# Performance work log

Hardware: AMD Instinct MI355X
Metric: run time of the kernel (lower is better)

The kernel has to match this reference:

```python
import jax, jax.numpy as jnp
import numpy as np

B, N_PER, P_PER = 64, 64, 2016   # graphs, nodes/graph, pairs/graph (C(64,2))
IN_DIM, HID, OUT = 64, 128, 10
EDGE_P = 0.125


def _build_graph_structures():
    """Integer preprocessing replicating build_2sets_from_embeddings's
    combinatorics (pairs, iso_type source, triangle-based 2-set edges)."""
    rng = np.random.default_rng(0)
    n, b = N_PER, B
    A = rng.random((b, n, n)) < EDGE_P
    A = np.triu(A, 1)
    A = A | A.transpose(0, 2, 1)                      # symmetric, no self loops
    gs, us, vs = np.nonzero(A)                        # directed edges, both dirs
    edge_index = np.stack([gs * n + us, gs * n + vs]).astype(np.int64)
    batch = np.repeat(np.arange(b), n).astype(np.int64)
    iu, iv = np.triu_indices(n, 1)                    # local pair (u<v) lists
    pidx = np.full((n, n), -1, np.int64)
    pidx[iu, iv] = np.arange(P_PER)
    pidx[iv, iu] = np.arange(P_PER)                   # symmetric lookup = sorted()
    pair_u = (np.arange(b)[:, None] * n + iu[None, :]).ravel().astype(np.int64)
    pair_v = (np.arange(b)[:, None] * n + iv[None, :]).ravel().astype(np.int64)
    iso_type = A[:, iu, iv].astype(np.float32).ravel()[:, None]  # [B*P_PER,1]
    # 2-set edges: pair (u,v) -> sorted(v,w) and sorted(u,w) for every common
    # neighbor w of u and v (matches _build_2set_edges exactly)
    common = A[:, iu, :] & A[:, iv, :]                # (B, P_PER, n)
    g2, ps, ws = np.nonzero(common)
    u, v = iu[ps], iv[ps]
    d1 = pidx[v, ws]
    d2 = pidx[u, ws]
    src = np.concatenate([g2 * P_PER + ps, g2 * P_PER + ps])
    dst = np.concatenate([g2 * P_PER + d1, g2 * P_PER + d2])
    two_edges = np.stack([src, dst]).astype(np.int64)
    two_batch = np.repeat(np.arange(b), P_PER).astype(np.int64)
    return edge_index, batch, pair_u, pair_v, iso_type, two_edges, two_batch


def setup_inputs() -> dict:
    ei, batch, pu, pv, iso, te, tb = _build_graph_structures()
    key = jax.random.key(0)
    ks = jax.random.split(key, 16)
    w = lambda k, i, o: jax.random.normal(k, (i, o), jnp.float32) / np.float32(np.sqrt(i))
    two_in = 2 * HID + 1
    return {
        "x": jax.random.normal(ks[0], (B * N_PER, IN_DIM), jnp.float32),
        "g1_W1_0": w(ks[1], IN_DIM, HID), "g1_W2_0": w(ks[2], IN_DIM, HID),
        "g1_W1_1": w(ks[3], HID, HID),    "g1_W2_1": w(ks[4], HID, HID),
        "g1_W1_2": w(ks[5], HID, HID),    "g1_W2_2": w(ks[6], HID, HID),
        "k_W1_0": w(ks[7], two_in, HID),  "k_W2_0": w(ks[8], two_in, HID),
        "k_W1_1": w(ks[9], HID, HID),     "k_W2_1": w(ks[10], HID, HID),
        "c_W0": w(ks[11], 2 * HID, HID),  "c_b0": jnp.zeros((HID,), jnp.float32),
        "c_W1": w(ks[12], HID, OUT),      "c_b1": jnp.zeros((OUT,), jnp.float32),
        "iso_type": jnp.asarray(iso),
        "edge_index": jnp.asarray(ei), "batch": jnp.asarray(batch),
        "pair_u": jnp.asarray(pu), "pair_v": jnp.asarray(pv),
        "two_edges": jnp.asarray(te), "two_batch": jnp.asarray(tb),
    }


def _mp_layer(h, ei, W1, W2):
    # relu( h @ W1 + scatter_add_{dst}( h[src] @ W2 ) )  -- OneGNNLayer / KSetLayer
    msg = h[ei[0]] @ W2
    agg = jax.ops.segment_sum(msg, ei[1], num_segments=h.shape[0])
    return jax.nn.relu(h @ W1 + agg)


def reference(x, g1_W1_0, g1_W2_0, g1_W1_1, g1_W2_1, g1_W1_2, g1_W2_2,
              k_W1_0, k_W2_0, k_W1_1, k_W2_1,
              c_W0, c_b0, c_W1, c_b1,
              iso_type, edge_index, batch, pair_u, pair_v, two_edges, two_batch):
    h = _mp_layer(x, edge_index, g1_W1_0, g1_W2_0)
    h = _mp_layer(h, edge_index, g1_W1_1, g1_W2_1)
    h = _mp_layer(h, edge_index, g1_W1_2, g1_W2_2)
    graph_emb_1 = jax.ops.segment_sum(h, batch, num_segments=B)
    # 2-set features: [h_u, h_v, iso_type]  -> [P, 2H+1]
    two_x = jnp.concatenate([h[pair_u], h[pair_v], iso_type], axis=1)
    h2 = _mp_layer(two_x, two_edges, k_W1_0, k_W2_0)
    h2 = _mp_layer(h2, two_edges, k_W1_1, k_W2_1)
    graph_emb_2 = jax.ops.segment_sum(h2, two_batch, num_segments=B)
    combined = jnp.concatenate([graph_emb_1, graph_emb_2], axis=1)
    hc = jax.nn.relu(combined @ c_W0 + c_b0)   # Dropout(p=0.5) inactive in eval
    return hc @ c_W1 + c_b1
```

## Files before the change

### kernel.cpp

```cpp
#include <hip/hip_runtime.h>
#include <hip/hip_bf16.h>


typedef short s16x8 __attribute__((ext_vector_type(8)));
typedef float f32x4 __attribute__((ext_vector_type(4)));

__device__ __forceinline__ unsigned short f2bf(float f) {
  union { float f; unsigned u; } x; x.f = f;
  unsigned r = (x.u + 0x7fffu + ((x.u >> 16) & 1u)) >> 16;
  return (unsigned short)r;
}
__device__ __forceinline__ float bf2f(unsigned short h) {
  union { unsigned u; float f; } x; x.u = ((unsigned)h) << 16;
  return x.f;
}
__device__ __forceinline__ float4 ldbf4(const unsigned short* p) {
  ushort4 q = *(const ushort4*)p;
  return make_float4(bf2f(q.x), bf2f(q.y), bf2f(q.z), bf2f(q.w));
}
__device__ __forceinline__ void stbf4(unsigned short* p, float4 v) {
  ushort4 q;
  q.x = f2bf(v.x); q.y = f2bf(v.y); q.z = f2bf(v.z); q.w = f2bf(v.w);
  *(ushort4*)p = q;
}
__device__ __forceinline__ float4 ld4(const float* p) { return *(const float4*)p; }

template<int KCS, int ASTR>
__device__ __forceinline__ void mfma_dual_lds(
    const unsigned short* A, const unsigned short* Wfrag,
    f32x4 (&accA)[8], f32x4 (&accB)[8])
{
  const int lane = threadIdx.x & 63;
  const int wv = threadIdx.x >> 6;
  const int row = wv * 16 + (lane & 15);
  const int k0 = (lane >> 4) << 3;
  const unsigned short* ap = A + row * ASTR + k0;
  const unsigned short* wp = Wfrag + (size_t)lane * 8;
#pragma unroll
  for (int i = 0; i < 8; ++i) { accA[i] = (f32x4)0.f; accB[i] = (f32x4)0.f; }
#pragma unroll
  for (int kc = 0; kc < KCS; ++kc) {
    s16x8 af = *(const s16x8*)(ap + kc * 32);
#pragma unroll
    for (int nt = 0; nt < 8; ++nt) {
      s16x8 b0 = *(const s16x8*)(wp + ((size_t)((nt)*KCS + kc) << 9));
      s16x8 b1 = *(const s16x8*)(wp + ((size_t)((8 + nt) * KCS + kc) << 9));
      accA[nt] = __builtin_amdgcn_mfma_f32_16x16x32_bf16(af, b0, accA[nt], 0, 0, 0);
      accB[nt] = __builtin_amdgcn_mfma_f32_16x16x32_bf16(af, b1, accB[nt], 0, 0, 0);
    }
  }
}

template<int KCS, int ASTR>
__device__ __forceinline__ void mfma_dual_lds16(
    const unsigned short* A, const unsigned short* Wfrag,
    f32x4 (&accA)[2], f32x4 (&accB)[2])
{
  const int lane = threadIdx.x & 63;
  const int w16 = threadIdx.x >> 6;
  const int rw = w16 & 3, ch = w16 >> 2;
  const int row = rw * 16 + (lane & 15);
  const int k0 = (lane >> 4) << 3;
  const unsigned short* ap = A + row * ASTR + k0;
  const unsigned short* wp = Wfrag + (size_t)lane * 8;
  accA[0] = (f32x4)0.f; accA[1] = (f32x4)0.f;
  accB[0] = (f32x4)0.f; accB[1] = (f32x4)0.f;
  __builtin_amdgcn_s_setprio(1);
#pragma unroll
  for (int kc = 0; kc < KCS; ++kc) {
    s16x8 af = *(const s16x8*)(ap + kc * 32);
#pragma unroll
    for (int n2 = 0; n2 < 2; ++n2) {
      int nt = ch * 2 + n2;
      s16x8 b0 = *(const s16x8*)(wp + ((size_t)(nt * KCS + kc) << 9));
      s16x8 b1 = *(const s16x8*)(wp + ((size_t)((8 + nt) * KCS + kc) << 9));
      accA[n2] = __builtin_amdgcn_mfma_f32_16x16x32_bf16(af, b0, accA[n2], 0, 0, 0);
      accB[n2] = __builtin_amdgcn_mfma_f32_16x16x32_bf16(af, b1, accB[n2], 0, 0, 0);
    }
  }
  __builtin_amdgcn_s_setprio(0);
}

__device__ __forceinline__ void epi_lds16(const f32x4 (&accA)[2], const f32x4 (&accB)[2],
    unsigned short (*preS)[136], unsigned short (*msgS)[136])
{
  const int lane = threadIdx.x & 63;
  const int w16 = threadIdx.x >> 6;
  const int rw = w16 & 3, ch = w16 >> 2;
  const int col = lane & 15;
  const int r0 = rw * 16 + ((lane >> 4) << 2);
  __syncthreads();
#pragma unroll
  for (int n2 = 0; n2 < 2; ++n2) {
    int nt = ch * 2 + n2;
#pragma unroll
    for (int r = 0; r < 4; ++r) {
      preS[r0 + r][nt * 16 + col] = f2bf(accA[n2][r]);
      msgS[r0 + r][nt * 16 + col] = f2bf(accB[n2][r]);
    }
  }
  __syncthreads();
}

__device__ __forceinline__ void epi_global(const f32x4 (&accA)[8], const f32x4 (&accB)[8],
    unsigned short (*sOut)[136], unsigned short* Ca, unsigned short* Cb, long tile)
{
  const int tid = threadIdx.x;
  const int lane = tid & 63;
  const int wv = tid >> 6;
  const int col = lane & 15;
  const int r0 = wv * 16 + ((lane >> 4) << 2);
  const long rowBase = tile * 64;
#pragma unroll
  for (int sel = 0; sel < 2; ++sel) {
    __syncthreads();
#pragma unroll
    for (int nt = 0; nt < 8; ++nt) {
#pragma unroll
      for (int r = 0; r < 4; ++r)
        sOut[r0 + r][nt * 16 + col] = f2bf(sel ? accB[nt][r] : accA[nt][r]);
    }
    __syncthreads();
    unsigned short* C = sel ? Cb : Ca;
#pragma unroll
    for (int i = 0; i < 4; ++i) {
      int fi = tid + i * 256;
      int row = fi >> 4;
      int c8 = fi & 15;
      *(uint4*)(C + (rowBase + row) * 128 + c8 * 8) = *(uint4*)&sOut[row][c8 * 8];
    }
  }
}

struct NArgs {
  const float* x;
  const int* ei;
  const int* gstart;
  const unsigned short *Wf0, *Wf1, *Wf2;
  unsigned short* Hn;
  float* ge1;
  int E1;
  const int* degP;
  int* bsumP;
  int P;
};

__global__ __launch_bounds__(1024) void node_plus(NArgs a)
{
  __shared__ __align__(16) unsigned short hS[64][136];
  __shared__ __align__(16) unsigned short preS[64][136];
  __shared__ __align__(16) unsigned short msgS[64][136];
  __shared__ int ldeg[64], lcur[64], loff[65];
  __shared__ unsigned short ledge[1024];
  __shared__ float sge[128];
  __shared__ int rs[1024];

  const int t = threadIdx.x;

  if ((int)blockIdx.x >= 64) {
    int chunk = blockIdx.x - 64;
    int idx = chunk * 1024 + t;
    rs[t] = (idx < a.P) ? a.degP[idx] : 0;
    __syncthreads();
    for (int d = 512; d > 0; d >>= 1) {
      if (t < d) rs[t] += rs[t + d];
      __syncthreads();
    }
    if (t == 0) a.bsumP[chunk] = rs[0];
    return;
  }

  const int b = blockIdx.x;
  const int base = b * 64;

  const int es = a.gstart[b], ee = a.gstart[b + 1];
  if (t < 64) ldeg[t] = 0;
  if (t < 128) sge[t] = 0.f;
  __syncthreads();
  for (int i = es + t; i < ee; i += 1024)
    atomicAdd(&ldeg[a.ei[a.E1 + i] - base], 1);
  __syncthreads();
  if (t < 64) {
    int v = ldeg[t], s = v;
#pragma unroll
    for (int d = 1; d < 64; d <<= 1) {
      int o = __shfl_up(s, d, 64);
      if (t >= d) s += o;
    }
    loff[t] = s - v;
    lcur[t] = s - v;
    if (t == 63) loff[64] = s;
  }
  unsigned short* xs = &preS[0][0];
  for (int i = t; i < 64 * 64; i += 1024) {
    int r = i >> 6, c = i & 63;
    xs[r * 72 + c] = f2bf(a.x[(size_t)(base + r) * 64 + c]);
  }
  __syncthreads();
  for (int i = es + t; i < ee; i += 1024) {
    int s = a.ei[i] - base, d = a.ei[a.E1 + i] - base;
    int pos = atomicAdd(&lcur[d], 1);
    ledge[pos] = (unsigned short)s;
  }
  __syncthreads();

  f32x4 accA[2], accB[2];
  const int grp = t >> 5, f = (t & 31) * 4;

  mfma_dual_lds16<2, 72>(xs, a.Wf0, accA, accB);
  epi_lds16(accA, accB, preS, msgS);
  for (int r = grp; r < 64; r += 32) {
    float4 acc = ldbf4(&preS[r][f]);
    int j1 = loff[r + 1];
    for (int j = loff[r]; j < j1; ++j) {
      float4 m = ldbf4(&msgS[ledge[j]][f]);
      acc.x += m.x; acc.y += m.y; acc.z += m.z; acc.w += m.w;
    }
    stbf4(&hS[r][f], make_float4(fmaxf(acc.x, 0.f), fmaxf(acc.y, 0.f),
                                 fmaxf(acc.z, 0.f), fmaxf(acc.w, 0.f)));
  }
  __syncthreads();

  mfma_dual_lds16<4, 136>(&hS[0][0], a.Wf1, accA, accB);
  epi_lds16(accA, accB, preS, msgS);
  for (int r = grp; r < 64; r += 32) {
    float4 acc = ldbf4(&preS[r][f]);
    int j1 = loff[r + 1];
    for (int j = loff[r]; j < j1; ++j) {
      float4 m = ldbf4(&msgS[ledge[j]][f]);
      acc.x += m.x; acc.y += m.y; acc.z += m.z; acc.w += m.w;
    }
    stbf4(&hS[r][f], make_float4(fmaxf(acc.x, 0.f), fmaxf(acc.y, 0.f),
                                 fmaxf(acc.z, 0.f), fmaxf(acc.w, 0.f)));
  }
  __syncthreads();

  mfma_dual_lds16<4, 136>(&hS[0][0], a.Wf2, accA, accB);
  epi_lds16(accA, accB, preS, msgS);
  {
    float4 g = make_float4(0.f, 0.f, 0.f, 0.f);
    for (int r = grp; r < 64; r += 32) {
      float4 acc = ldbf4(&preS[r][f]);
      int j1 = loff[r + 1];
      for (int j = loff[r]; j < j1; ++j) {
        float4 m = ldbf4(&msgS[ledge[j]][f]);
        acc.x += m.x; acc.y += m.y; acc.z += m.z; acc.w += m.w;
      }
      float4 o = make_float4(fmaxf(acc.x, 0.f), fmaxf(acc.y, 0.f),
                             fmaxf(acc.z, 0.f), fmaxf(acc.w, 0.f));
      stbf4(&hS[r][f], o);
      g.x += o.x; g.y += o.y; g.z += o.z; g.w += o.w;
    }
    atomicAdd(&sge[f + 0], g.x);
    atomicAdd(&sge[f + 1], g.y);
    atomicAdd(&sge[f + 2], g.z);
    atomicAdd(&sge[f + 3], g.w);
  }
  __syncthreads();
  if (t < 128) a.ge1[b * 128 + t] = sge[t];
  {
    int row = t >> 4, c8 = t & 15;
    *(uint4*)(a.Hn + (size_t)(base + row) * 128 + c8 * 8) = *(uint4*)&hS[row][c8 * 8];
  }
}

struct HArgs {
  const unsigned short* Hn;
  const unsigned short *Wf3, *Wf4;
  unsigned short *HU1, *HU2, *HV1, *HV2;
  const int* degP;
  const int* bsumP;
  int* offP; int* curP;
  int P; int nb;
};

__global__ __launch_bounds__(256) void hv_plus(HArgs a)
{
  __shared__ __align__(16) unsigned short hS[64][136];
  __shared__ int s[256];
  __shared__ int basePfx;
  const int tid = threadIdx.x;

  if ((int)blockIdx.x >= 128) {
    int b = blockIdx.x - 128;
    int t = tid;
    if (t == 0) {
      int acc = 0;
      for (int k = 0; k < b; ++k) acc += a.bsumP[k];
      basePfx = acc;
    }
    int base = b * 1024 + t * 4;
    int v0 = 0, v1 = 0, v2 = 0, v3 = 0;
    if (base + 0 < a.P) v0 = a.degP[base + 0];
    if (base + 1 < a.P) v1 = a.degP[base + 1];
    if (base + 2 < a.P) v2 = a.degP[base + 2];
    if (base + 3 < a.P) v3 = a.degP[base + 3];
    s[t] = v0 + v1 + v2 + v3;
    __syncthreads();
    for (int d = 1; d < 256; d <<= 1) {
      int v = (t >= d) ? s[t - d] : 0;
      __syncthreads();
      s[t] += v;
      __syncthreads();
    }
    int run = basePfx + ((t == 0) ? 0 : s[t - 1]);
    if (base + 0 < a.P) { a.offP[base + 0] = run; a.curP[base + 0] = run; run += v0; }
    if (base + 1 < a.P) { a.offP[base + 1] = run; a.curP[base + 1] = run; run += v1; }
    if (base + 2 < a.P) { a.offP[base + 2] = run; a.curP[base + 2] = run; run += v2; }
    if (base + 3 < a.P) { a.offP[base + 3] = run; a.curP[base + 3] = run; run += v3; }
    if (b == a.nb - 1 && t == 0) a.offP[a.P] = basePfx + a.bsumP[b];
    return;
  }

  const int g = blockIdx.x >> 1;
  const int sel = blockIdx.x & 1;
  const unsigned short* src = a.Hn + (size_t)g * 64 * 128;
#pragma unroll
  for (int i = 0; i < 4; ++i) {
    int fi = tid + i * 256;
    int row = fi >> 4, c8 = fi & 15;
    *(uint4*)&hS[row][c8 * 8] = *(const uint4*)(src + row * 128 + c8 * 8);
  }
  __syncthreads();
  f32x4 accA[8], accB[8];
  mfma_dual_lds<4, 136>(&hS[0][0], sel ? a.Wf4 : a.Wf3, accA, accB);
  epi_global(accA, accB, hS, sel ? a.HV1 : a.HU1, sel ? a.HV2 : a.HU2, g);
}

struct PrepArgs {
  const float* wa[6];
  const float* wb[6];
  unsigned short* Wf[6];
  const int* te; int E2;
  int* degP;
  const int* ei; int E1;
  int* gstart;
  int nCnt;
};

__global__ void prep(PrepArgs p)
{
  int bb = blockIdx.x, t = threadIdx.x;
  if (bb < 88) {
    int gid = bb * 256 + t;
    if (gid < 22528) {
      int pi, local, kcs, kclog;
      if (gid < 2048) { pi = 0; local = gid; kcs = 2; kclog = 1; }
      else { int r = gid - 2048; pi = 1 + (r >> 12); local = r & 4095; kcs = 4; kclog = 2; }
      int lane = local & 63;
      int t1 = local >> 6;
      int kc = t1 & (kcs - 1);
      int t2 = t1 >> kclog;
      int nt = t2 & 7;
      int wsel = t2 >> 3;
      const float* W = wsel ? p.wb[pi] : p.wa[pi];
      int k0 = kc * 32 + ((lane >> 4) << 3);
      int n = nt * 16 + (lane & 15);
      unsigned short tmp[8];
#pragma unroll
      for (int j = 0; j < 8; ++j) tmp[j] = f2bf(W[(size_t)(k0 + j) * 128 + n]);
      *(uint4*)(p.Wf[pi] + (size_t)local * 8) = *(uint4*)tmp;
    }
  } else if (bb < 88 + p.nCnt) {
    int e = (bb - 88) * 256 + t;
    if (e < p.E2) atomicAdd(&p.degP[p.te[p.E2 + e]], 1);
  } else {
    int e = (bb - 88 - p.nCnt) * 256 + t;
    if (e <= p.E1) {
      int ge = (e < p.E1) ? (p.ei[e] >> 6) : 64;
      int gp = (e > 0) ? (p.ei[e - 1] >> 6) : -1;
      for (int g = gp + 1; g <= ge; ++g) p.gstart[g] = e;
    }
  }
}

__global__ void csr_fill_pair(const int* __restrict__ te, int E2,
                              const int* __restrict__ pu, const int* __restrict__ pv,
                              const float* __restrict__ iso,
                              int* __restrict__ curP, int4* __restrict__ recP)
{
  int e = blockIdx.x * 256 + threadIdx.x;
  if (e >= E2) return;
  int s = te[e], d = te[E2 + e];
  int pos = atomicAdd(&curP[d], 1);
  recP[pos] = make_int4(pu[s], pv[s], __float_as_int(iso[s]), s);
}

__global__ __launch_bounds__(256) void gather_two0_bf(
    const unsigned short* __restrict__ HU1, const unsigned short* __restrict__ HV1,
    const unsigned short* __restrict__ HU2, const unsigned short* __restrict__ HV2,
    const float* __restrict__ iso,
    const float* __restrict__ w1iso, const float* __restrict__ w2iso,
    const int* __restrict__ pu, const int* __restrict__ pv,
    const int* __restrict__ off, const int4* __restrict__ rec,
    unsigned short* __restrict__ out, int P)
{
  int blk = (int)blockIdx.x;
  const int nB = (int)gridDim.x;
  if ((nB & 7) == 0)
    blk = (blk & 7) * (nB >> 3) + (blk >> 3);
  int p = blk * 8 + (threadIdx.x >> 5);
  if (p >= P) return;
  int f = (threadIdx.x & 31) * 4;
  float4 wi1 = ld4(w1iso + f);
  float4 wi2 = ld4(w2iso + f);
  int u0 = pu[p], v0 = pv[p];
  float is0 = iso[p];
  float4 a = ldbf4(HU1 + (size_t)u0 * 128 + f);
  float4 b = ldbf4(HV1 + (size_t)v0 * 128 + f);
  float4 acc;
  acc.x = a.x + b.x + is0 * wi1.x;
  acc.y = a.y + b.y + is0 * wi1.y;
  acc.z = a.z + b.z + is0 * wi1.z;
  acc.w = a.w + b.w + is0 * wi1.w;
  int j = off[p], e1 = off[p + 1];
  for (; j + 1 < e1; j += 2) {
    int4 r0 = rec[j], r1 = rec[j + 1];
    float4 mu0 = ldbf4(HU2 + (size_t)r0.x * 128 + f);
    float4 mv0 = ldbf4(HV2 + (size_t)r0.y * 128 + f);
    float4 mu1 = ldbf4(HU2 + (size_t)r1.x * 128 + f);
    float4 mv1 = ldbf4(HV2 + (size_t)r1.y * 128 + f);
    float i0 = __int_as_float(r0.z), i1 = __int_as_float(r1.z);
    acc.x += mu0.x + mv0.x + i0 * wi2.x + mu1.x + mv1.x + i1 * wi2.x;
    acc.y += mu0.y + mv0.y + i0 * wi2.y + mu1.y + mv1.y + i1 * wi2.y;
    acc.z += mu0.z + mv0.z + i0 * wi2.z + mu1.z + mv1.z + i1 * wi2.z;
    acc.w += mu0.w + mv0.w + i0 * wi2.w + mu1.w + mv1.w + i1 * wi2.w;
  }
  if (j < e1) {
    int4 r0 = rec[j];
    float4 mu0 = ldbf4(HU2 + (size_t)r0.x * 128 + f);
    float4 mv0 = ldbf4(HV2 + (size_t)r0.y * 128 + f);
    float i0 = __int_as_float(r0.z);
    acc.x += mu0.x + mv0.x + i0 * wi2.x;
    acc.y += mu0.y + mv0.y + i0 * wi2.y;
    acc.z += mu0.z + mv0.z + i0 * wi2.z;
    acc.w += mu0.w + mv0.w + i0 * wi2.w;
  }
  stbf4(out + (size_t)p * 128 + f,
        make_float4(fmaxf(acc.x, 0.f), fmaxf(acc.y, 0.f),
                    fmaxf(acc.z, 0.f), fmaxf(acc.w, 0.f)));
}

__global__ __launch_bounds__(64) void pair_l1(
    const unsigned short* __restrict__ H2,
    const unsigned short* __restrict__ Wfrag,
    const int* __restrict__ off, const int4* __restrict__ rec,
    float* __restrict__ gep)
{
  __shared__ __align__(16) unsigned short hS[16][136];
  __shared__ int offS[17];
  __shared__ int recwS[256];
  __shared__ float sge[128];

  const int tid = threadIdx.x;
  int qt = (int)blockIdx.x;
  const int nB = (int)gridDim.x;
  if ((nB & 7) == 0)
    qt = (qt & 7) * (nB >> 3) + (qt >> 3);
  const int r0 = qt * 16;

  if (tid < 17) offS[tid] = off[r0 + tid];
  sge[tid] = 0.f;
  sge[tid + 64] = 0.f;

  {
    const unsigned short* src = H2 + (size_t)r0 * 128;
#pragma unroll
    for (int i = 0; i < 4; ++i) {
      int fi = tid + i * 64;
      int row = fi >> 4, c8 = fi & 15;
      *(uint4*)&hS[row][c8 * 8] = *(const uint4*)(src + row * 128 + c8 * 8);
    }
  }
  __syncthreads();

  const int e0 = offS[0];
  const int ecnt = offS[16] - e0;
  const bool useS = (ecnt <= 256);
  if (useS)
    for (int j = tid; j < ecnt; j += 64) recwS[j] = rec[e0 + j].w;

  const int lane = tid;
  const int arow = lane & 15;
  const int k0 = (lane >> 4) << 3;
  const unsigned short* hp = &hS[0][0] + arow * 136 + k0;
  const unsigned short* wp = Wfrag + (size_t)lane * 8;
  f32x4 acc[8];
#pragma unroll
  for (int nt = 0; nt < 8; ++nt) acc[nt] = (f32x4)0.f;
  __builtin_amdgcn_s_setprio(1);
#pragma unroll
  for (int kc = 0; kc < 4; ++kc) {
    s16x8 ah = *(const s16x8*)(hp + kc * 32);
#pragma unroll
    for (int nt = 0; nt < 8; ++nt) {
      s16x8 b0 = *(const s16x8*)(wp + ((size_t)(nt * 4 + kc) << 9));
      acc[nt] = __builtin_amdgcn_mfma_f32_16x16x32_bf16(ah, b0, acc[nt], 0, 0, 0);
    }
  }
  __builtin_amdgcn_s_setprio(0);
  __syncthreads();

  {
    const int grp = tid >> 5, f = (tid & 31) * 4;
    for (int i = grp; i < 16; i += 2) {
      float4 a = make_float4(0.f, 0.f, 0.f, 0.f);
      int j = offS[i], e1 = offS[i + 1];
      for (; j + 1 < e1; j += 2) {
        int s0 = useS ? recwS[j - e0] : rec[j].w;
        int s1 = useS ? recwS[j + 1 - e0] : rec[j + 1].w;
        float4 m0 = ldbf4(H2 + (size_t)s0 * 128 + f);
        float4 m1 = ldbf4(H2 + (size_t)s1 * 128 + f);
        a.x += m0.x + m1.x; a.y += m0.y + m1.y;
        a.z += m0.z + m1.z; a.w += m0.w + m1.w;
      }
      if (j < e1) {
        int s0 = useS ? recwS[j - e0] : rec[j].w;
        float4 m0 = ldbf4(H2 + (size_t)s0 * 128 + f);
        a.x += m0.x; a.y += m0.y; a.z += m0.z; a.w += m0.w;
      }
      stbf4(&hS[i][f], a);
    }
  }
  __syncthreads();

  __builtin_amdgcn_s_setprio(1);
#pragma unroll
  for (int kc = 0; kc < 4; ++kc) {
    s16x8 ag = *(const s16x8*)(hp + kc * 32);
#pragma unroll
    for (int nt = 0; nt < 8; ++nt) {
      s16x8 b1 = *(const s16x8*)(wp + ((size_t)((8 + nt) * 4 + kc) << 9));
      acc[nt] = __builtin_amdgcn_mfma_f32_16x16x32_bf16(ag, b1, acc[nt], 0, 0, 0);
    }
  }
  __builtin_amdgcn_s_setprio(0);

  const int col0 = lane & 15;
#pragma unroll
  for (int nt = 0; nt < 8; ++nt) {
    float s = fmaxf(acc[nt][0], 0.f) + fmaxf(acc[nt][1], 0.f)
            + fmaxf(acc[nt][2], 0.f) + fmaxf(acc[nt][3], 0.f);
    atomicAdd(&sge[nt * 16 + col0], s);
  }
  __syncthreads();
  gep[(size_t)qt * 128 + tid] = sge[tid];
  gep[(size_t)qt * 128 + tid + 64] = sge[tid + 64];
}

__global__ void classifier(const float* __restrict__ ge1, const float* __restrict__ gep,
                           const float* __restrict__ W0, const float* __restrict__ b0,
                           const float* __restrict__ W1, const float* __restrict__ b1,
                           float* __restrict__ out)
{
  __shared__ float comb[256];
  __shared__ float hc[128];
  int g = blockIdx.x, t = threadIdx.x;
  comb[t] = ge1[g * 128 + t];
  float s2 = 0.f;
  const float* gpr = gep + (size_t)g * 126 * 128 + t;
  for (int i = 0; i < 126; ++i) s2 += gpr[i * 128];
  comb[t + 128] = s2;
  __syncthreads();
  float s = b0[t];
  for (int k = 0; k < 256; ++k) s += comb[k] * W0[k * 128 + t];
  hc[t] = fmaxf(s, 0.f);
  __syncthreads();
  if (t < 10) {
    float s2o = b1[t];
    for (int k = 0; k < 128; ++k) s2o += hc[k] * W1[k * 10 + t];
    out[g * 10 + t] = s2o;
  }
}

extern "C" void kernel_launch(void* const* d_in, const int* in_sizes, int n_in,
                              void* d_out, int out_size, void* d_ws, size_t ws_size,
                              hipStream_t stream)
{
  (void)n_in; (void)out_size; (void)ws_size;
  const float* x       = (const float*)d_in[0];
  const float* g1_W1_0 = (const float*)d_in[1];
  const float* g1_W2_0 = (const float*)d_in[2];
  const float* g1_W1_1 = (const float*)d_in[3];
  const float* g1_W2_1 = (const float*)d_in[4];
  const float* g1_W1_2 = (const float*)d_in[5];
  const float* g1_W2_2 = (const float*)d_in[6];
  const float* k_W1_0  = (const float*)d_in[7];
  const float* k_W2_0  = (const float*)d_in[8];
  const float* k_W1_1  = (const float*)d_in[9];
  const float* k_W2_1  = (const float*)d_in[10];
  const float* c_W0    = (const float*)d_in[11];
  const float* c_b0    = (const float*)d_in[12];
  const float* c_W1    = (const float*)d_in[13];
  const float* c_b1    = (const float*)d_in[14];
  const float* iso     = (const float*)d_in[15];
  const int*   ei      = (const int*)d_in[16];
  const int*   pu      = (const int*)d_in[18];
  const int*   pv      = (const int*)d_in[19];
  const int*   te      = (const int*)d_in[20];

  const int N  = in_sizes[0] / 64;
  const int E1 = in_sizes[16] / 2;
  const int P  = in_sizes[18];
  const int E2 = in_sizes[20] / 2;
  const int B  = 64;
  const int nTiles = P / 64;

  const size_t NH = (size_t)N * 128;
  const size_t PH = (size_t)P * 128;

  float* ge1 = (float*)d_ws;
  float* gep = ge1 + 8192;
  unsigned short* HU1 = (unsigned short*)(gep + (size_t)4 * nTiles * 128);
  unsigned short* HV1 = HU1 + NH;
  unsigned short* HU2 = HV1 + NH;
  unsigned short* HV2 = HU2 + NH;
  unsigned short* H2   = HV2 + NH;
  unsigned short* Hn   = H2 + PH;
  unsigned short* Wf0  = Hn + NH;
  unsigned short* Wf1  = Wf0 + 16384;
  unsigned short* Wf2  = Wf1 + 32768;
  unsigned short* Wf3  = Wf2 + 32768;
  unsigned short* Wf4  = Wf3 + 32768;
  unsigned short* Wf5  = Wf4 + 32768;

  size_t ipOff = ((size_t)((char*)(Wf5 + 32768) - (char*)d_ws) + 15) & ~(size_t)15;
  int4* recP   = (int4*)((char*)d_ws + ipOff);
  int* degP    = (int*)(recP + E2);
  int* offP    = degP + P;
  int* curP    = offP + P + 1;
  int* bsumP   = curP + P;
  int* gstartN = bsumP + 128;

  const int nbP  = (P + 1023) / 1024;
  const int nCnt = (E2 + 255) / 256;
  const int nBnd = (E1 + 256) / 256;

  hipMemsetAsync(degP, 0, (size_t)P * 4, stream);

  PrepArgs pa;
  pa.wa[0] = g1_W1_0;           pa.wb[0] = g1_W2_0;
  pa.wa[1] = g1_W1_1;           pa.wb[1] = g1_W2_1;
  pa.wa[2] = g1_W1_2;           pa.wb[2] = g1_W2_2;
  pa.wa[3] = k_W1_0;            pa.wb[3] = k_W2_0;
  pa.wa[4] = k_W1_0 + 128*128;  pa.wb[4] = k_W2_0 + 128*128;
  pa.wa[5] = k_W1_1;            pa.wb[5] = k_W2_1;
  pa.Wf[0] = Wf0; pa.Wf[1] = Wf1; pa.Wf[2] = Wf2;
  pa.Wf[3] = Wf3; pa.Wf[4] = Wf4; pa.Wf[5] = Wf5;
  pa.te = te; pa.E2 = E2; pa.degP = degP;
  pa.ei = ei; pa.E1 = E1; pa.gstart = gstartN; pa.nCnt = nCnt;
  prep<<<88 + nCnt + nBnd, 256, 0, stream>>>(pa);

  NArgs na;
  na.x = x; na.ei = ei; na.gstart = gstartN; na.E1 = E1;
  na.Wf0 = Wf0; na.Wf1 = Wf1; na.Wf2 = Wf2;
  na.Hn = Hn; na.ge1 = ge1;
  na.degP = degP; na.bsumP = bsumP; na.P = P;
  node_plus<<<B + nbP, 1024, 0, stream>>>(na);

  HArgs ha;
  ha.Hn = Hn; ha.Wf3 = Wf3; ha.Wf4 = Wf4;
  ha.HU1 = HU1; ha.HU2 = HU2; ha.HV1 = HV1; ha.HV2 = HV2;
  ha.degP = degP; ha.bsumP = bsumP; ha.offP = offP; ha.curP = curP;
  ha.P = P; ha.nb = nbP;
  hv_plus<<<2 * B + nbP, 256, 0, stream>>>(ha);

  csr_fill_pair<<<nCnt, 256, 0, stream>>>(te, E2, pu, pv, iso, curP, recP);

  gather_two0_bf<<<(P + 7) / 8, 256, 0, stream>>>(HU1, HV1, HU2, HV2, iso,
                                                  k_W1_0 + 256 * 128, k_W2_0 + 256 * 128,
                                                  pu, pv, offP, recP, H2, P);

  pair_l1<<<nTiles * 4, 64, 0, stream>>>(H2, Wf5, offP, recP, gep);

  classifier<<<B, 128, 0, stream>>>(ge1, gep, c_W0, c_b0, c_W1, c_b1, (float*)d_out);
}
```

Measured before the change: 268.7 us.

## Fuse classifier into pair_l1 via last-block atomic reduction; shrink gather blocks

Removes the separate classifier launch. Each pair_l1 tile now atomically adds its partial graph embedding into a per-graph ge2 buffer, and the last tile of each graph (found with an atomic counter) runs the two-layer classifier for that graph. The gather_two0_bf kernel also moves from 256-thread to 64-thread blocks with two pairs per block. The fusion saves a launch and the partial-sum buffer pass, but adds global atomics, threadfences and a serial classifier tail on 126 tiles' worth of work per graph.

```diff
diff --git a/kernel.cpp b/kernel.cpp
--- a/kernel.cpp
+++ b/kernel.cpp
@@ -386,7 +386,7 @@
   recP[pos] = make_int4(pu[s], pv[s], __float_as_int(iso[s]), s);
 }
 
-__global__ __launch_bounds__(256) void gather_two0_bf(
+__global__ __launch_bounds__(64) void gather_two0_bf(
     const unsigned short* __restrict__ HU1, const unsigned short* __restrict__ HV1,
     const unsigned short* __restrict__ HU2, const unsigned short* __restrict__ HV2,
     const float* __restrict__ iso,
@@ -399,7 +399,7 @@
   const int nB = (int)gridDim.x;
   if ((nB & 7) == 0)
     blk = (blk & 7) * (nB >> 3) + (blk >> 3);
-  int p = blk * 8 + (threadIdx.x >> 5);
+  int p = blk * 2 + (threadIdx.x >> 5);
   if (p >= P) return;
   int f = (threadIdx.x & 31) * 4;
   float4 wi1 = ld4(w1iso + f);
@@ -441,16 +441,24 @@
                     fmaxf(acc.z, 0.f), fmaxf(acc.w, 0.f)));
 }
 
-__global__ __launch_bounds__(64) void pair_l1(
-    const unsigned short* __restrict__ H2,
-    const unsigned short* __restrict__ Wfrag,
-    const int* __restrict__ off, const int4* __restrict__ rec,
-    float* __restrict__ gep)
+struct PArgs {
+  const unsigned short* H2;
+  const unsigned short* Wfrag;
+  const int* off; const int4* rec;
+  float* ge2;
+  int* cnt;
+  const float* ge1;
+  const float *cW0, *cb0, *cW1, *cb1;
+  float* out;
+};
+
+__global__ __launch_bounds__(64) void pair_l1(PArgs a)
 {
   __shared__ __align__(16) unsigned short hS[16][136];
   __shared__ int offS[17];
   __shared__ int recwS[256];
   __shared__ float sge[128];
+  __shared__ int isLast;
 
   const int tid = threadIdx.x;
   int qt = (int)blockIdx.x;
@@ -459,12 +467,12 @@
     qt = (qt & 7) * (nB >> 3) + (qt >> 3);
   const int r0 = qt * 16;
 
-  if (tid < 17) offS[tid] = off[r0 + tid];
+  if (tid < 17) offS[tid] = a.off[r0 + tid];
   sge[tid] = 0.f;
   sge[tid + 64] = 0.f;
 
   {
-    const unsigned short* src = H2 + (size_t)r0 * 128;
+    const unsigned short* src = a.H2 + (size_t)r0 * 128;
 #pragma unroll
     for (int i = 0; i < 4; ++i) {
       int fi = tid + i * 64;
@@ -478,13 +486,13 @@
   const int ecnt = offS[16] - e0;
   const bool useS = (ecnt <= 256);
   if (useS)
-    for (int j = tid; j < ecnt; j += 64) recwS[j] = rec[e0 + j].w;
+    for (int j = tid; j < ecnt; j += 64) recwS[j] = a.rec[e0 + j].w;
 
   const int lane = tid;
   const int arow = lane & 15;
   const int k0 = (lane >> 4) << 3;
   const unsigned short* hp = &hS[0][0] + arow * 136 + k0;
-  const unsigned short* wp = Wfrag + (size_t)lane * 8;
+  const unsigned short* wp = a.Wfrag + (size_t)lane * 8;
   f32x4 acc[8];
 #pragma unroll
   for (int nt = 0; nt < 8; ++nt) acc[nt] = (f32x4)0.f;
@@ -504,22 +512,22 @@
   {
     const int grp = tid >> 5, f = (tid & 31) * 4;
     for (int i = grp; i < 16; i += 2) {
-      float4 a = make_float4(0.f, 0.f, 0.f, 0.f);
+      float4 g4 = make_float4(0.f, 0.f, 0.f, 0.f);
       int j = offS[i], e1 = offS[i + 1];
       for (; j + 1 < e1; j += 2) {
-        int s0 = useS ? recwS[j - e0] : rec[j].w;
-        int s1 = useS ? recwS[j + 1 - e0] : rec[j + 1].w;
-        float4 m0 = ldbf4(H2 + (size_t)s0 * 128 + f);
-        float4 m1 = ldbf4(H2 + (size_t)s1 * 128 + f);
-        a.x += m0.x + m1.x; a.y += m0.y + m1.y;
-        a.z += m0.z + m1.z; a.w += m0.w + m1.w;
+        int s0 = useS ? recwS[j - e0] : a.rec[j].w;
+        int s1 = useS ? recwS[j + 1 - e0] : a.rec[j + 1].w;
+        float4 m0 = ldbf4(a.H2 + (size_t)s0 * 128 + f);
+        float4 m1 = ldbf4(a.H2 + (size_t)s1 * 128 + f);
+        g4.x += m0.x + m1.x; g4.y += m0.y + m1.y;
+        g4.z += m0.z + m1.z; g4.w += m0.w + m1.w;
       }
       if (j < e1) {
-        int s0 = useS ? recwS[j - e0] : rec[j].w;
-        float4 m0 = ldbf4(H2 + (size_t)s0 * 128 + f);
-        a.x += m0.x; a.y += m0.y; a.z += m0.z; a.w += m0.w;
+        int s0 = useS ? recwS[j - e0] : a.rec[j].w;
+        float4 m0 = ldbf4(a.H2 + (size_t)s0 * 128 + f);
+        g4.x += m0.x; g4.y += m0.y; g4.z += m0.z; g4.w += m0.w;
       }
-      stbf4(&hS[i][f], a);
+      stbf4(&hS[i][f], g4);
     }
   }
   __syncthreads();
@@ -544,32 +552,36 @@
     atomicAdd(&sge[nt * 16 + col0], s);
   }
   __syncthreads();
-  gep[(size_t)qt * 128 + tid] = sge[tid];
-  gep[(size_t)qt * 128 + tid + 64] = sge[tid + 64];
-}
-
-__global__ void classifier(const float* __restrict__ ge1, const float* __restrict__ gep,
-                           const float* __restrict__ W0, const float* __restrict__ b0,
-                           const float* __restrict__ W1, const float* __restrict__ b1,
-                           float* __restrict__ out)
-{
-  __shared__ float comb[256];
-  __shared__ float hc[128];
-  int g = blockIdx.x, t = threadIdx.x;
-  comb[t] = ge1[g * 128 + t];
-  float s2 = 0.f;
-  const float* gpr = gep + (size_t)g * 126 * 128 + t;
-  for (int i = 0; i < 126; ++i) s2 += gpr[i * 128];
-  comb[t + 128] = s2;
-  __syncthreads();
-  float s = b0[t];
-  for (int k = 0; k < 256; ++k) s += comb[k] * W0[k * 128 + t];
-  hc[t] = fmaxf(s, 0.f);
-  __syncthreads();
-  if (t < 10) {
-    float s2o = b1[t];
-    for (int k = 0; k < 128; ++k) s2o += hc[k] * W1[k * 10 + t];
-    out[g * 10 + t] = s2o;
+
+  const int g = qt / 126;
+  atomicAdd(&a.ge2[g * 128 + tid], sge[tid]);
+  atomicAdd(&a.ge2[g * 128 + tid + 64], sge[tid + 64]);
+  __threadfence();
+  if (tid == 0) {
+    int old = atomicAdd(&a.cnt[g], 1);
+    isLast = (old == 125);
+  }
+  __syncthreads();
+  if (!isLast) return;
+  __threadfence();
+
+  float* comb = (float*)&hS[0][0];
+  float* hc = comb + 256;
+  for (int i = tid; i < 128; i += 64) {
+    comb[i] = a.ge1[g * 128 + i];
+    comb[128 + i] = atomicAdd(&a.ge2[g * 128 + i], 0.0f);
+  }
+  __syncthreads();
+  for (int h = tid; h < 128; h += 64) {
+    float s = a.cb0[h];
+    for (int k = 0; k < 256; ++k) s += comb[k] * a.cW0[k * 128 + h];
+    hc[h] = fmaxf(s, 0.f);
+  }
+  __syncthreads();
+  if (tid < 10) {
+    float s2 = a.cb1[tid];
+    for (int k = 0; k < 128; ++k) s2 += hc[k] * a.cW1[k * 10 + tid];
+    a.out[g * 10 + tid] = s2;
   }
 }
 
@@ -610,8 +622,7 @@
   const size_t PH = (size_t)P * 128;
 
   float* ge1 = (float*)d_ws;
-  float* gep = ge1 + 8192;
-  unsigned short* HU1 = (unsigned short*)(gep + (size_t)4 * nTiles * 128);
+  unsigned short* HU1 = (unsigned short*)(ge1 + 8192);
   unsigned short* HV1 = HU1 + NH;
   unsigned short* HU2 = HV1 + NH;
   unsigned short* HV2 = HU2 + NH;
@@ -627,7 +638,9 @@
   size_t ipOff = ((size_t)((char*)(Wf5 + 32768) - (char*)d_ws) + 15) & ~(size_t)15;
   int4* recP   = (int4*)((char*)d_ws + ipOff);
   int* degP    = (int*)(recP + E2);
-  int* offP    = degP + P;
+  float* ge2   = (float*)(degP + P);
+  int* cntP    = (int*)(ge2 + 8192);
+  int* offP    = cntP + 64;
   int* curP    = offP + P + 1;
   int* bsumP   = curP + P;
   int* gstartN = bsumP + 128;
@@ -636,7 +649,7 @@
   const int nCnt = (E2 + 255) / 256;
   const int nBnd = (E1 + 256) / 256;
 
-  hipMemsetAsync(degP, 0, (size_t)P * 4, stream);
+  hipMemsetAsync(degP, 0, (size_t)(P + 8192 + 64) * 4, stream);
 
   PrepArgs pa;
   pa.wa[0] = g1_W1_0;           pa.wb[0] = g1_W2_0;
@@ -667,11 +680,14 @@
 
   csr_fill_pair<<<nCnt, 256, 0, stream>>>(te, E2, pu, pv, iso, curP, recP);
 
-  gather_two0_bf<<<(P + 7) / 8, 256, 0, stream>>>(HU1, HV1, HU2, HV2, iso,
-                                                  k_W1_0 + 256 * 128, k_W2_0 + 256 * 128,
-                                                  pu, pv, offP, recP, H2, P);
-
-  pair_l1<<<nTiles * 4, 64, 0, stream>>>(H2, Wf5, offP, recP, gep);
-
-  classifier<<<B, 128, 0, stream>>>(ge1, gep, c_W0, c_b0, c_W1, c_b1, (float*)d_out);
-}
+  gather_two0_bf<<<P / 2, 64, 0, stream>>>(HU1, HV1, HU2, HV2, iso,
+                                           k_W1_0 + 256 * 128, k_W2_0 + 256 * 128,
+                                           pu, pv, offP, recP, H2, P);
+
+  PArgs pga;
+  pga.H2 = H2; pga.Wfrag = Wf5; pga.off = offP; pga.rec = recP;
+  pga.ge2 = ge2; pga.cnt = cntP; pga.ge1 = ge1;
+  pga.cW0 = c_W0; pga.cb0 = c_b0; pga.cW1 = c_W1; pga.cb1 = c_b1;
+  pga.out = (float*)d_out;
+  pair_l1<<<nTiles * 4, 64, 0, stream>>>(pga);
+}
```

After: 403.6 us. 1.5x slower.
